# Optimization experiments

Measured on AMD Instinct MI355X. Metric: run time of the kernel, lower is better.

Reference implementation:

```python
import jax, jax.numpy as jnp
import numpy as np

BATCH = 50000
MULS = (256, 256, 128)   # multiplicities of 0e, 1o, 2e
DIMS = (1, 3, 5)         # irrep dims (2l+1)
TOTAL = sum(m * d for m, d in zip(MULS, DIMS))  # 1664
# path_normalization='element', gradient_normalization='path' with one
# instruction per output irrep => path_weight = sqrt(1/mul_in), weight_std = 1
PATH_W = tuple(np.float32(1.0 / np.sqrt(m)) for m in MULS)


def setup_inputs() -> dict:
    key = jax.random.key(0)
    k = jax.random.split(key, 4)
    x = jax.random.normal(k[0], (BATCH, TOTAL), dtype=jnp.float32)
    w0 = jax.random.normal(k[1], (MULS[0], MULS[0]), dtype=jnp.float32)
    w1 = jax.random.normal(k[2], (MULS[1], MULS[1]), dtype=jnp.float32)
    w2 = jax.random.normal(k[3], (MULS[2], MULS[2]), dtype=jnp.float32)
    return {"x": x, "w0": w0, "w1": w1, "w2": w2}


def reference(x, w0, w1, w2):
    # For each irrep block: reshape to [B, mul, ir_dim], contract mul with the
    # per-instruction weight ('uw,ui->wi' batched), scale by path_weight,
    # and place into the corresponding output slice (here: concatenate).
    ws = (w0, w1, w2)
    out_blocks = []
    off = 0
    for w, mul, dim, pw in zip(ws, MULS, DIMS, PATH_W):
        seg = x[:, off:off + mul * dim].reshape(-1, mul, dim)  # [B, u, i]
        y = pw * jnp.einsum('uw,bui->bwi', w, seg)             # [B, w, i]
        out_blocks.append(y.reshape(x.shape[0], mul * dim))
        off += mul * dim
    return jnp.concatenate(out_blocks, axis=-1)  # [B, 1664]
```

## Files before the change

### kernel.cpp

```cpp
#include <hip/hip_runtime.h>


typedef __attribute__((ext_vector_type(8))) short short8;
typedef __attribute__((ext_vector_type(4))) float f32x4;

#define NBATCH 50000
#define NTOTAL 1664
#define NTILES 3125
#define GRIDX  1042

__device__ __forceinline__ unsigned short f2bf(float f) {
    union { float f; unsigned u; } v; v.f = f;
    unsigned r = v.u + 0x7fffu + ((v.u >> 16) & 1u);
    return (unsigned short)(r >> 16);
}

__global__ void prep_kernel(const float* __restrict__ w0,
                            const float* __restrict__ w1,
                            const float* __restrict__ w2,
                            unsigned short* __restrict__ ws) {
    int e = blockIdx.x * blockDim.x + threadIdx.x;
    const float* W; int N, base;
    if (e < 65536)       { W = w0; N = 256; base = 0; }
    else if (e < 131072) { W = w1; N = 256; base = 65536;  e -= 65536; }
    else if (e < 147456) { W = w2; N = 128; base = 131072; e -= 131072; }
    else return;
    int j = e & 7;
    int lane = (e >> 3) & 63;
    int qt = e >> 9;
    int NT = N >> 4;
    int t = qt % NT;
    int q = qt / NT;
    int u = q * 32 + ((lane >> 4) << 3) + j;
    int w = t * 16 + (lane & 15);
    ws[base + e] = f2bf(W[u * N + w]);
}

template<int D, int K, int NT, int NTW, int OFF>
__device__ __forceinline__ void run_block(const float* __restrict__ x,
                                          float* __restrict__ out,
                                          const short8* __restrict__ bsw,
                                          float pw, char* __restrict__ sm,
                                          int tile) {
    constexpr int COLS   = K * D;
    constexpr int C4     = COLS / 4;
    constexpr int RB     = COLS * 2;
    constexpr int ROUNDS = (16 * C4) / 256;

    const int tid  = threadIdx.x;
    const int lane = tid & 63;
    const int wave = tid >> 6;

    float4 pf[ROUNDS];
    auto ld_pf = [&](int t) {
#pragma unroll
        for (int rr = 0; rr < ROUNDS; ++rr) {
            int c    = rr * 256 + tid;
            int row  = c / C4;
            int col4 = c - row * C4;
            pf[rr] = *((const float4*)
                       (x + (size_t)(t * 16 + row) * NTOTAL + OFF) + col4);
        }
    };
    auto cvt_write = [&]() {
#pragma unroll
        for (int rr = 0; rr < ROUNDS; ++rr) {
            int c    = rr * 256 + tid;
            int row  = c / C4;
            int col4 = c - row * C4;
            float4 v = pf[rr];
            unsigned long long pk =
                  (unsigned long long)f2bf(v.x)
                | ((unsigned long long)f2bf(v.y) << 16)
                | ((unsigned long long)f2bf(v.z) << 32)
                | ((unsigned long long)f2bf(v.w) << 48);
            *(unsigned long long*)(sm + row * RB
                                   + ((col4 * 8) ^ ((row & 7) << 4))) = pk;
        }
    };

    ld_pf(tile);
    cvt_write();
    __syncthreads();

    const int bcol = lane & 15;
    const int quad = lane >> 4;
    const char* lrow = sm + bcol * RB;
    const int sw = (bcol & 7) << 4;

    while (true) {
        f32x4 acc[NTW][D];
#pragma unroll
        for (int tt = 0; tt < NTW; ++tt)
#pragma unroll
            for (int i = 0; i < D; ++i)
                acc[tt][i] = (f32x4){0.f, 0.f, 0.f, 0.f};

#pragma unroll
        for (int q = 0; q < K / 32; ++q) {
            const int cb = (q * 32 + quad * 8) * D * 2;
            short8 raw[D];
#pragma unroll
            for (int m = 0; m < D; ++m)
                raw[m] = *(const short8*)(lrow + ((cb + m * 16) ^ sw));

            short8 af[D];
#pragma unroll
            for (int i = 0; i < D; ++i)
#pragma unroll
                for (int j = 0; j < 8; ++j) {
                    const int e = j * D + i;
                    af[i][j] = raw[e >> 3][e & 7];
                }

#pragma unroll
            for (int tt = 0; tt < NTW; ++tt) {
                const int tw = wave * NTW + tt;
                short8 bf = bsw[(q * NT + tw) * 64 + lane];
#pragma unroll
                for (int i = 0; i < D; ++i)
                    acc[tt][i] = __builtin_amdgcn_mfma_f32_16x16x32_bf16(
                        af[i], bf, acc[tt][i], 0, 0, 0);
            }
        }

        const int nxt  = tile + GRIDX;
        const bool more = nxt < NTILES;

        __builtin_amdgcn_sched_barrier(0);
        if (more) ld_pf(nxt);
        __builtin_amdgcn_sched_barrier(0);

        const int b0 = tile << 4;
#pragma unroll
        for (int tt = 0; tt < NTW; ++tt) {
            const int wcol = (wave * NTW + tt) * 16 + bcol;
#pragma unroll
            for (int r = 0; r < 4; ++r) {
                float* op = out + (size_t)(b0 + quad * 4 + r) * NTOTAL + OFF
                            + wcol * D;
#pragma unroll
                for (int i = 0; i < D; ++i)
                    op[i] = acc[tt][i][r] * pw;
            }
        }

        if (!more) break;

        asm volatile("s_waitcnt lgkmcnt(0)" ::: "memory");
        __builtin_amdgcn_s_barrier();
        __builtin_amdgcn_sched_barrier(0);

        cvt_write();
        __syncthreads();
        tile = nxt;
    }
}

__global__ __launch_bounds__(256)
void linear_kernel(const float* __restrict__ x, float* __restrict__ out,
                   const unsigned short* __restrict__ ws) {
    __shared__ __attribute__((aligned(16))) char sm[49152];
    const short8* bs0 = (const short8*)(ws);
    const short8* bs1 = (const short8*)(ws + 65536);
    const short8* bs2 = (const short8*)(ws + 131072);
    if (blockIdx.y == 0)
        run_block<1, 256, 16, 4, 0>(x, out, bs0, 0.0625f, sm, blockIdx.x);
    else if (blockIdx.y == 1)
        run_block<3, 256, 16, 4, 256>(x, out, bs1, 0.0625f, sm, blockIdx.x);
    else
        run_block<5, 128, 8, 2, 1024>(x, out, bs2, 0.08838834764831845f, sm,
                                      blockIdx.x);
}

extern "C" void kernel_launch(void* const* d_in, const int* in_sizes, int n_in,
                              void* d_out, int out_size, void* d_ws,
                              size_t ws_size, hipStream_t stream) {
    const float* x  = (const float*)d_in[0];
    const float* w0 = (const float*)d_in[1];
    const float* w1 = (const float*)d_in[2];
    const float* w2 = (const float*)d_in[3];
    unsigned short* ws = (unsigned short*)d_ws;

    prep_kernel<<<dim3(576), 256, 0, stream>>>(w0, w1, w2, ws);

    dim3 grid(GRIDX, 3);
    linear_kernel<<<grid, 256, 0, stream>>>(x, (float*)d_out, ws);
}
```

Baseline: 560.3 us.

## Use persistent 1024-thread blocks with register-resident weights and per-irrep CU split

Replaces the 1042x3 grid of 256-thread blocks with 256 persistent 1024-thread workgroups. Each irrep block gets a fixed share of workgroups (40/118/98), roughly matched to its work. Each wave now owns one 16-column weight tile and keeps it in registers for the whole run, so B fragments are no longer reloaded from global memory on every tile. The l=2 block processes 32 rows per iteration split across two half-groups, with tail guards for the batch edge. The prefetch of the next tile is moved before the MFMA loop to overlap loads with compute. The trade-off is more register pressure from waves_per_eu(4,4), and the hardcoded workgroup split may leave some CUs idle or unbalanced.

```diff
diff --git a/kernel.cpp b/kernel.cpp
--- a/kernel.cpp
+++ b/kernel.cpp
@@ -6,8 +6,6 @@
 
 #define NBATCH 50000
 #define NTOTAL 1664
-#define NTILES 3125
-#define GRIDX  1042
 
 __device__ __forceinline__ unsigned short f2bf(float f) {
     union { float f; unsigned u; } v; v.f = f;
@@ -36,36 +34,50 @@
     ws[base + e] = f2bf(W[u * N + w]);
 }
 
-template<int D, int K, int NT, int NTW, int OFF>
+template<int D, int K, int NT, int OFF, int HALVES>
 __device__ __forceinline__ void run_block(const float* __restrict__ x,
                                           float* __restrict__ out,
                                           const short8* __restrict__ bsw,
                                           float pw, char* __restrict__ sm,
-                                          int tile) {
+                                          int wgidx, int nwg) {
     constexpr int COLS   = K * D;
     constexpr int C4     = COLS / 4;
     constexpr int RB     = COLS * 2;
-    constexpr int ROUNDS = (16 * C4) / 256;
+    constexpr int ROWS   = 16 * HALVES;
+    constexpr int ROUNDS = (ROWS * C4) / 1024;
+    constexpr int QMAX   = K / 32;
+    constexpr int NITER  = (NBATCH + ROWS - 1) / ROWS;
 
     const int tid  = threadIdx.x;
     const int lane = tid & 63;
-    const int wave = tid >> 6;
+    const int w    = tid >> 6;
+    const int tw   = (HALVES == 2) ? (w & (NT - 1)) : w;
+    const int half = (HALVES == 2) ? (w >> 3) : 0;
 
     float4 pf[ROUNDS];
-    auto ld_pf = [&](int t) {
+    auto ld_pf = [&](int rb) {
 #pragma unroll
         for (int rr = 0; rr < ROUNDS; ++rr) {
-            int c    = rr * 256 + tid;
+            int c    = rr * 1024 + tid;
             int row  = c / C4;
             int col4 = c - row * C4;
-            pf[rr] = *((const float4*)
-                       (x + (size_t)(t * 16 + row) * NTOTAL + OFF) + col4);
+            int gr   = rb + row;
+            if constexpr (HALVES == 2) {
+                if (gr < NBATCH)
+                    pf[rr] = *((const float4*)
+                               (x + (size_t)gr * NTOTAL + OFF) + col4);
+                else
+                    pf[rr] = (float4){0.f, 0.f, 0.f, 0.f};
+            } else {
+                pf[rr] = *((const float4*)
+                           (x + (size_t)gr * NTOTAL + OFF) + col4);
+            }
         }
     };
     auto cvt_write = [&]() {
 #pragma unroll
         for (int rr = 0; rr < ROUNDS; ++rr) {
-            int c    = rr * 256 + tid;
+            int c    = rr * 1024 + tid;
             int row  = c / C4;
             int col4 = c - row * C4;
             float4 v = pf[rr];
@@ -79,25 +91,35 @@
         }
     };
 
-    ld_pf(tile);
-    cvt_write();
-    __syncthreads();
+    short8 breg[QMAX];
+#pragma unroll
+    for (int q = 0; q < QMAX; ++q)
+        breg[q] = bsw[(q * NT + tw) * 64 + lane];
+
+    int it = wgidx;
+    ld_pf(it * ROWS);
 
     const int bcol = lane & 15;
     const int quad = lane >> 4;
-    const char* lrow = sm + bcol * RB;
+    const char* lrow = sm + (half * 16 + bcol) * RB;
     const int sw = (bcol & 7) << 4;
 
     while (true) {
-        f32x4 acc[NTW][D];
+        cvt_write();
+        __syncthreads();
+
+        const int nxt  = it + nwg;
+        const bool more = nxt < NITER;
+        if (more) ld_pf(nxt * ROWS);
+        __builtin_amdgcn_sched_barrier(0);
+
+        f32x4 acc[D];
 #pragma unroll
-        for (int tt = 0; tt < NTW; ++tt)
-#pragma unroll
-            for (int i = 0; i < D; ++i)
-                acc[tt][i] = (f32x4){0.f, 0.f, 0.f, 0.f};
+        for (int i = 0; i < D; ++i)
+            acc[i] = (f32x4){0.f, 0.f, 0.f, 0.f};
 
 #pragma unroll
-        for (int q = 0; q < K / 32; ++q) {
+        for (int q = 0; q < QMAX; ++q) {
             const int cb = (q * 32 + quad * 8) * D * 2;
             short8 raw[D];
 #pragma unroll
@@ -114,35 +136,23 @@
                 }
 
 #pragma unroll
-            for (int tt = 0; tt < NTW; ++tt) {
-                const int tw = wave * NTW + tt;
-                short8 bf = bsw[(q * NT + tw) * 64 + lane];
-#pragma unroll
-                for (int i = 0; i < D; ++i)
-                    acc[tt][i] = __builtin_amdgcn_mfma_f32_16x16x32_bf16(
-                        af[i], bf, acc[tt][i], 0, 0, 0);
-            }
+            for (int i = 0; i < D; ++i)
+                acc[i] = __builtin_amdgcn_mfma_f32_16x16x32_bf16(
+                    af[i], breg[q], acc[i], 0, 0, 0);
         }
 
-        const int nxt  = tile + GRIDX;
-        const bool more = nxt < NTILES;
-
-        __builtin_amdgcn_sched_barrier(0);
-        if (more) ld_pf(nxt);
-        __builtin_amdgcn_sched_barrier(0);
-
-        const int b0 = tile << 4;
+        const int b0   = it * ROWS + half * 16;
+        const int wcol = tw * 16 + bcol;
 #pragma unroll
-        for (int tt = 0; tt < NTW; ++tt) {
-            const int wcol = (wave * NTW + tt) * 16 + bcol;
+        for (int r = 0; r < 4; ++r) {
+            const int grow = b0 + quad * 4 + r;
+            if constexpr (HALVES == 2) {
+                if (grow >= NBATCH) continue;
+            }
+            float* op = out + (size_t)grow * NTOTAL + OFF + wcol * D;
 #pragma unroll
-            for (int r = 0; r < 4; ++r) {
-                float* op = out + (size_t)(b0 + quad * 4 + r) * NTOTAL + OFF
-                            + wcol * D;
-#pragma unroll
-                for (int i = 0; i < D; ++i)
-                    op[i] = acc[tt][i][r] * pw;
-            }
+            for (int i = 0; i < D; ++i)
+                op[i] = acc[i][r] * pw;
         }
 
         if (!more) break;
@@ -150,27 +160,26 @@
         asm volatile("s_waitcnt lgkmcnt(0)" ::: "memory");
         __builtin_amdgcn_s_barrier();
         __builtin_amdgcn_sched_barrier(0);
-
-        cvt_write();
-        __syncthreads();
-        tile = nxt;
+        it = nxt;
     }
 }
 
-__global__ __launch_bounds__(256)
+__global__ __attribute__((amdgpu_waves_per_eu(4, 4)))
+__launch_bounds__(1024, 4)
 void linear_kernel(const float* __restrict__ x, float* __restrict__ out,
                    const unsigned short* __restrict__ ws) {
-    __shared__ __attribute__((aligned(16))) char sm[49152];
+    __shared__ __attribute__((aligned(16))) char sm[40960];
     const short8* bs0 = (const short8*)(ws);
     const short8* bs1 = (const short8*)(ws + 65536);
     const short8* bs2 = (const short8*)(ws + 131072);
-    if (blockIdx.y == 0)
-        run_block<1, 256, 16, 4, 0>(x, out, bs0, 0.0625f, sm, blockIdx.x);
-    else if (blockIdx.y == 1)
-        run_block<3, 256, 16, 4, 256>(x, out, bs1, 0.0625f, sm, blockIdx.x);
+    const int b = blockIdx.x;
+    if (b < 40)
+        run_block<1, 256, 16, 0, 1>(x, out, bs0, 0.0625f, sm, b, 40);
+    else if (b < 158)
+        run_block<3, 256, 16, 256, 1>(x, out, bs1, 0.0625f, sm, b - 40, 118);
     else
-        run_block<5, 128, 8, 2, 1024>(x, out, bs2, 0.08838834764831845f, sm,
-                                      blockIdx.x);
+        run_block<5, 128, 8, 1024, 2>(x, out, bs2, 0.08838834764831845f, sm,
+                                      b - 158, 98);
 }
 
 extern "C" void kernel_launch(void* const* d_in, const int* in_sizes, int n_in,
@@ -184,6 +193,5 @@
 
     prep_kernel<<<dim3(576), 256, 0, stream>>>(w0, w1, w2, ws);
 
-    dim3 grid(GRIDX, 3);
-    linear_kernel<<<grid, 256, 0, stream>>>(x, (float*)d_out, ws);
+    linear_kernel<<<dim3(256), 1024, 0, stream>>>(x, (float*)d_out, ws);
 }
```

Result: faster. 544.7 us (-2.8%).
